# Kernel optimization log

Measured on AMD Instinct MI355X. Metric: run time of the kernel, lower is better.

Reference implementation:

```python
import jax, jax.numpy as jnp
import numpy as np

V = 8000      # output_size (vocab)
EMB = 256     # emb_size
ENC = 512     # enc_hid_size
DEC = 512     # dec_hid_size
HE = 20       # energizer hidden (fixed in source)


def setup_inputs() -> dict:
    key = jax.random.key(0)
    ks = jax.random.split(key, 12)
    B, S, T = 64, 128, 128
    s = 0.05
    return {
        "enc_hid": jax.random.normal(ks[0], (B, S, ENC), dtype=jnp.float32),
        "real_output": jax.random.randint(ks[1], (B, T), 0, V),
        "W_e1": jax.random.normal(ks[2], (ENC + DEC, HE), dtype=jnp.float32) * s,
        "b_e1": jnp.zeros((HE,), jnp.float32),
        "W_e2": jax.random.normal(ks[3], (HE, 1), dtype=jnp.float32) * s,
        "b_e2": jnp.zeros((1,), jnp.float32),
        "emb": jax.random.normal(ks[4], (V, EMB), dtype=jnp.float32) * s,
        "W_rnn": jax.random.normal(ks[5], (EMB + DEC + ENC, DEC), dtype=jnp.float32) * s,
        "b_rnn": jnp.zeros((DEC,), jnp.float32),
        "W_out": jax.random.normal(ks[6], (EMB + DEC + ENC, V), dtype=jnp.float32) * s,
        "b_out": jnp.zeros((V,), jnp.float32),
    }


def _decode(enc_hid, real_output, W_e1, b_e1, W_e2, b_e2, emb, W_rnn, b_rnn, W_out, b_out):
    B, S, _ = enc_hid.shape

    def step(carry, y_i):
        last_char, last_hidden = carry  # [B] int, [B,DEC]
        # additive attention, vectorized over all encoder positions
        hid_b = jnp.broadcast_to(last_hidden[:, None, :], (B, S, DEC))
        cat = jnp.concatenate([enc_hid, hid_b], axis=-1)          # [B,S,ENC+DEC]
        e = jax.nn.elu(cat @ W_e1 + b_e1)                          # [B,S,HE]
        e = jax.nn.elu(e @ W_e2 + b_e2)[..., 0]                    # [B,S]
        ew = jnp.exp(e)
        w = ew / jnp.sum(ew, axis=1, keepdims=True)                # [B,S]
        context = jnp.einsum('bs,bse->be', w, enc_hid)             # [B,ENC]
        last_ch = emb[last_char % V]                               # [B,EMB]
        new_hidden = jax.nn.elu(
            jnp.concatenate([last_ch, last_hidden, context], axis=1) @ W_rnn + b_rnn)
        out = jax.nn.elu(
            jnp.concatenate([last_ch, new_hidden, context], axis=1) @ W_out + b_out)
        # teacher_forcing_prob = 1.0 -> next char is the ground truth token
        return (y_i, new_hidden), (out, w)

    init = (jnp.zeros((B,), real_output.dtype), jnp.zeros((B, DEC), enc_hid.dtype))
    _, (outs, weights) = jax.lax.scan(step, init, real_output.T)   # [T,B,V], [T,B,S]
    return outs.transpose(1, 0, 2), weights.transpose(1, 0, 2)


def reference(enc_hid, real_output, W_e1, b_e1, W_e2, b_e2, emb, W_rnn, b_rnn, W_out, b_out):
    return _decode(enc_hid, real_output, W_e1, b_e1, W_e2, b_e2, emb,
                   W_rnn, b_rnn, W_out, b_out)
```

## Files before the change

### kernel.cpp

```cpp
#include <hip/hip_runtime.h>
#include <hip/hip_bf16.h>
#include <stdint.h>

#define BATCH 64
#define SLEN 128
#define TLEN 128
#define ENCD 512
#define DECD 512
#define EMBD 256
#define VOC  8000
#define HE   20
#define KX   1280
#define NPAD 8064

typedef __attribute__((ext_vector_type(8))) short short8;
typedef __attribute__((ext_vector_type(8))) _Float16 half8v;
typedef __attribute__((ext_vector_type(4))) float f32x4;
typedef _Float16 h2 __attribute__((ext_vector_type(2)));

__device__ inline unsigned short f2bf(float f) {
  union { float f; uint32_t u; } v; v.f = f;
  uint32_t r = v.u + 0x7fff + ((v.u >> 16) & 1);
  return (unsigned short)(r >> 16);
}
__device__ inline unsigned short f16bits(float f) {
  union { _Float16 h; unsigned short u; } c; c.h = (_Float16)f; return c.u;
}
__device__ inline uint32_t pkh2(float a, float b) {
  union { h2 h; uint32_t u; } v;
  v.h = h2{(_Float16)a, (_Float16)b};
  return v.u;
}
__device__ inline float fdot2(uint32_t a, uint32_t b, float c) {
#if __has_builtin(__builtin_amdgcn_fdot2)
  union { uint32_t u; h2 h; } x, y; x.u = a; y.u = b;
  return __builtin_amdgcn_fdot2(x.h, y.h, c, false);
#else
  union { uint32_t u; h2 h; } x, y; x.u = a; y.u = b;
  return c + (float)x.h[0] * (float)y.h[0] + (float)x.h[1] * (float)y.h[1];
#endif
}
__device__ inline float eluf(float x) { return x > 0.f ? x : (expf(x) - 1.f); }

typedef const __attribute__((address_space(1))) unsigned int* gptr_t;
typedef __attribute__((address_space(3))) unsigned int* lptr_t;
__device__ inline void gload16(const void* g, void* l) {
  __builtin_amdgcn_global_load_lds((gptr_t)g, (lptr_t)l, 16, 0, 0);
}

__global__ __launch_bounds__(256) void k_e1(const float* __restrict__ enc,
                                            const float* __restrict__ We1,
                                            float* __restrict__ E1) {
  __shared__ float rowbuf[4][ENCD];
  __shared__ float part[4][HE][2];
  int r0 = blockIdx.x * 4;
  int tid = threadIdx.x;
  for (int i = tid; i < 4 * ENCD; i += 256) {
    int rl = i >> 9, e = i & 511;
    rowbuf[rl][e] = enc[(size_t)(r0 + rl) * ENCD + e];
  }
  __syncthreads();
  if (tid < 160) {
    int kg = tid / 80, rem = tid % 80, rl = rem / 20, h = rem % 20;
    float acc = 0.f;
    for (int k = kg * 256; k < kg * 256 + 256; ++k)
      acc += rowbuf[rl][k] * We1[k * HE + h];
    part[rl][h][kg] = acc;
  }
  __syncthreads();
  if (tid < 80) {
    int rl = tid / 20, h = tid % 20;
    int r = r0 + rl, bb = r >> 7, ss = r & 127;
    E1[((size_t)bb * HE + h) * SLEN + ss] = part[rl][h][0] + part[rl][h][1];
  }
}

__global__ __launch_bounds__(256) void k_tr_wout(const float* __restrict__ Wo,
                                                 unsigned short* __restrict__ WoT) {
  __shared__ float tile[64][65];
  int n0 = blockIdx.x * 64, k0 = blockIdx.y * 64;
  int tid = threadIdx.x;
  for (int i = tid; i < 4096; i += 256) {
    int kk = i >> 6, nn = i & 63;
    int n = n0 + nn;
    tile[kk][nn] = (n < VOC) ? Wo[(size_t)(k0 + kk) * VOC + n] : 0.f;
  }
  __syncthreads();
  for (int i = tid; i < 4096; i += 256) {
    int nn = i >> 6, kk = i & 63;
    WoT[(size_t)(n0 + nn) * KX + k0 + kk] = f2bf(tile[kk][nn]);
  }
}

__global__ __launch_bounds__(256) void k_tr_w(const float* __restrict__ src,
                                              unsigned short* __restrict__ dst,
                                              int k0, int KN, int fmt) {
  __shared__ float tile[64][65];
  int n0 = blockIdx.x * 64, kt = blockIdx.y * 64;
  int tid = threadIdx.x;
  for (int i = tid; i < 4096; i += 256) {
    int kk = i >> 6, nn = i & 63;
    tile[kk][nn] = src[(size_t)(k0 + kt + kk) * 512 + n0 + nn];
  }
  __syncthreads();
  for (int i = tid; i < 4096; i += 256) {
    int nn = i >> 6, kk = i & 63;
    float v = tile[kk][nn];
    dst[(size_t)(n0 + nn) * KN + kt + kk] = fmt ? f2bf(v) : f16bits(v);
  }
}

__global__ __launch_bounds__(256) void k_prep_wr(const float* __restrict__ Wr,
                                                 unsigned short* __restrict__ W2) {
  int i = blockIdx.x * 256 + threadIdx.x;
  int n = i & 511;
  int j = (i >> 9) & 7;
  int kc = (i >> 12) & 31;
  int h = (i >> 17) & 1;
  int k = h * 256 + kc * 8 + j;
  W2[(((size_t)(h * 32 + kc) * 512) + n) * 8 + j] = f16bits(Wr[(size_t)(256 + k) * 512 + n]);
}

__global__ __launch_bounds__(256) void k_ench(const float* __restrict__ enc,
                                              unsigned short* __restrict__ ench) {
  int i = (blockIdx.x * 256 + threadIdx.x) * 4;
  float4 v = *(const float4*)(enc + i);
  ushort4 o = { f16bits(v.x), f16bits(v.y), f16bits(v.z), f16bits(v.w) };
  *(ushort4*)(ench + i) = o;
}

__global__ __launch_bounds__(256) void k_wh(const float* __restrict__ wout,
                                            unsigned short* __restrict__ wh) {
  int i = (blockIdx.x * 256 + threadIdx.x) * 4;
  float4 v = *(const float4*)(wout + i);
  ushort4 o = { f16bits(v.x), f16bits(v.y), f16bits(v.z), f16bits(v.w) };
  *(ushort4*)(wh + i) = o;
}

__global__ __launch_bounds__(256) void k_tr_encb(const float* __restrict__ enc,
                                                 unsigned short* __restrict__ encT) {
  __shared__ float tile[64][65];
  int b = blockIdx.x, e0 = blockIdx.y * 64, s0 = blockIdx.z * 64;
  int tid = threadIdx.x;
  const float* eb = enc + (size_t)b * SLEN * ENCD;
  for (int i = tid; i < 4096; i += 256) {
    int ss = i >> 6, ee = i & 63;
    tile[ss][ee] = eb[(size_t)(s0 + ss) * ENCD + e0 + ee];
  }
  __syncthreads();
  unsigned short* ob = encT + (size_t)b * ENCD * SLEN;
  for (int i = tid; i < 4096; i += 256) {
    int ee = i >> 6, ss = i & 63;
    ob[(size_t)(e0 + ee) * SLEN + s0 + ss] = f16bits(tile[ss][ee]);
  }
}

__global__ __launch_bounds__(256) void k_lc(const int* __restrict__ ro,
                                            const float* __restrict__ emb,
                                            unsigned short* __restrict__ X) {
  int r = blockIdx.x;
  int t = r >> 6, b = r & 63;
  int lc = (t == 0) ? 0 : ro[b * TLEN + t - 1];
  lc = ((lc % VOC) + VOC) % VOC;
  X[(size_t)r * KX + threadIdx.x] = f2bf(emb[(size_t)lc * EMBD + threadIdx.x]);
}

#define BM 128
#define BN 128
#define BK 64

template<int MODE>
__global__ __launch_bounds__(256) void k_gs(
    const unsigned short* __restrict__ A,
    const unsigned short* __restrict__ B,
    const float* __restrict__ bias,
    unsigned short* __restrict__ Cout)
{
  constexpr int As = (MODE == 0) ? KX : (MODE == 1 ? 512 : 128);
  constexpr int Bs = (MODE == 0) ? 256 : (MODE == 1 ? 512 : 128);
  constexpr int KT = (MODE == 0) ? 4 : (MODE == 1 ? 8 : 2);
  __shared__ __align__(16) unsigned short Asd[BM * BK];
  __shared__ __align__(16) unsigned short Bsd[BN * BK];
  int bx = blockIdx.x, by = blockIdx.y;
  int tid = threadIdx.x;
  int wid = tid >> 6, lane = tid & 63;
  int wr = wid >> 1, wc = wid & 1;

  f32x4 acc[4][4];
  for (int i = 0; i < 4; ++i)
    for (int j = 0; j < 4; ++j) acc[i][j] = (f32x4)0.f;

  const unsigned short* Abase = A + (size_t)by * BM * As;
  const unsigned short* Bbase = B + (size_t)bx * BN * Bs + (MODE == 2 ? (size_t)by * 512 * 128 : 0);

  for (int kt = 0; kt < KT; ++kt) {
    for (int j = 0; j < 4; ++j) {
      int c = tid + j * 256;
      int r = c >> 3, c16 = c & 7;
      int sk = c16 ^ (r & 7);
      gload16(Abase + (size_t)r * As + kt * BK + sk * 8, (char*)Asd + c * 16);
      gload16(Bbase + (size_t)r * Bs + kt * BK + sk * 8, (char*)Bsd + c * 16);
    }
    __syncthreads();
    for (int ks = 0; ks < 2; ++ks) {
      short8 af[4], bf[4];
      int kc = ks * 4 + (lane >> 4);
      for (int i = 0; i < 4; ++i) {
        int r = wr * 64 + i * 16 + (lane & 15);
        af[i] = *(const short8*)((const char*)Asd + r * 128 + ((kc ^ (r & 7)) * 16));
      }
      for (int j = 0; j < 4; ++j) {
        int r = wc * 64 + j * 16 + (lane & 15);
        bf[j] = *(const short8*)((const char*)Bsd + r * 128 + ((kc ^ (r & 7)) * 16));
      }
      for (int i = 0; i < 4; ++i)
        for (int j = 0; j < 4; ++j) {
          if constexpr (MODE == 0)
            acc[i][j] = __builtin_amdgcn_mfma_f32_16x16x32_bf16(af[i], bf[j], acc[i][j], 0, 0, 0);
          else
            acc[i][j] = __builtin_amdgcn_mfma_f32_16x16x32_f16(
                __builtin_bit_cast(half8v, af[i]), __builtin_bit_cast(half8v, bf[j]), acc[i][j], 0, 0, 0);
        }
    }
    __syncthreads();
  }

  int rl = lane >> 4, cl = lane & 15;
  for (int j = 0; j < 4; ++j) {
    int gn = bx * BN + wc * 64 + j * 16 + cl;
    for (int i = 0; i < 4; ++i) {
      for (int q = 0; q < 4; ++q) {
        int gm = by * BM + wr * 64 + i * 16 + rl * 4 + q;
        float v = acc[i][j][q];
        if constexpr (MODE == 0) {
          Cout[(size_t)gm * 512 + gn] = f16bits(v + bias[gn]);
        } else if constexpr (MODE == 1) {
          int bb = gm >> 7, s = gm & 127;
          Cout[(((size_t)(bb * 16 + (s >> 3)) * 512) + gn) * 8 + (s & 7)] = f16bits(v);
        } else {
          int tt = gm & 127, bb = gm >> 7;
          Cout[((size_t)tt * 64 + bb) * KX + 768 + gn] = f2bf(v);
        }
      }
    }
  }
}

__global__ __launch_bounds__(1024) void k_recur(
    const float* __restrict__ We1,
    const float* __restrict__ be1,
    const float* __restrict__ We2,
    const float* __restrict__ be2,
    const uint4* __restrict__ W2,
    const uint4* __restrict__ encW2,
    const unsigned short* __restrict__ Remb,
    const float* __restrict__ E1g,
    unsigned short* __restrict__ X,
    float* __restrict__ wout)
{
  __shared__ __align__(16) uint4 el[16][512];
  __shared__ uint32_t E1p[HE][SLEN / 2];
  __shared__ uint32_t w1p[HE][257];
  __shared__ uint32_t hpair[DECD / 2];
  __shared__ uint32_t wpairS[SLEN / 2];
  __shared__ float ph[2][DECD];
  __shared__ float be1s[HE], w2s[HE];
  __shared__ float be2s;

  int b = blockIdx.x, tid = threadIdx.x;

  for (int i = tid; i < 16 * 512; i += 1024) ((uint4*)el)[i] = encW2[(size_t)b * 8192 + i];
  for (int i = tid; i < HE * (SLEN / 2); i += 1024) {
    int h = i >> 6, p = i & 63;
    const float* ebase = E1g + ((size_t)b * HE + h) * SLEN;
    ((uint32_t*)E1p)[i] = pkh2(ebase[2 * p], ebase[2 * p + 1]);
  }
  for (int i = tid; i < HE * 256; i += 1024) {
    int h = i >> 8, p = i & 255;
    w1p[h][p] = pkh2(We1[(size_t)(ENCD + 2 * p) * HE + h],
                     We1[(size_t)(ENCD + 2 * p + 1) * HE + h]);
  }
  for (int i = tid; i < DECD / 2; i += 1024) hpair[i] = 0;
  for (int i = tid; i < DECD; i += 1024) { ph[0][i] = 0.f; ph[1][i] = 0.f; }
  if (tid < HE) { be1s[tid] = be1[tid]; w2s[tid] = We2[tid]; }
  if (tid == 0) be2s = be2[0];
  __syncthreads();

  const int lane = tid & 63;
  const bool attn_wave = (tid >= 960);
  int mn, mh0, mblocks;
  if (tid < 448)      { mn = tid;              mh0 = 0; mblocks = 4; }
  else if (tid < 896) { mn = tid - 448;        mh0 = 1; mblocks = 4; }
  else if (tid < 960) { mn = 448 + (tid - 896); mh0 = 0; mblocks = 8; }
  else                { mn = 0;                mh0 = 0; mblocks = 0; }
  const uint4* Wp = W2 + (size_t)(mh0 * 32) * 512 + mn;
  const uint4* hp4 = (const uint4*)hpair;
  const int hbase = mh0 * 32;

  int ah = lane % 20, aseg = lane / 20;
  int q0 = aseg * 86;
  int q1 = (aseg == 2) ? 256 : q0 + 86;
  if (aseg >= 3) { q0 = 0; q1 = 0; }

  for (int t = 0; t < TLEN; ++t) {
    const int rowr = t * BATCH + b;
    float rpre = 0.f;

    if (!attn_wave) {
      if (tid < 512) {
        union { unsigned short u; _Float16 f; } c;
        c.u = Remb[(size_t)rowr * 512 + tid];
        rpre = (float)c.f;
      }
      float a0 = 0, a1 = 0, a2 = 0, a3 = 0;
      uint4 cb[8], nb[8];
      #pragma unroll
      for (int j = 0; j < 8; ++j) cb[j] = Wp[(size_t)j * 512];
      for (int blk = 0; blk < mblocks; ++blk) {
        if (blk + 1 < mblocks) {
          #pragma unroll
          for (int j = 0; j < 8; ++j) nb[j] = Wp[(size_t)((blk + 1) * 8 + j) * 512];
        }
        #pragma unroll
        for (int j = 0; j < 8; ++j) {
          uint4 wv = cb[j]; uint4 xv = hp4[hbase + blk * 8 + j];
          a0 = fdot2(wv.x, xv.x, a0); a1 = fdot2(wv.y, xv.y, a1);
          a2 = fdot2(wv.z, xv.z, a2); a3 = fdot2(wv.w, xv.w, a3);
        }
        #pragma unroll
        for (int j = 0; j < 8; ++j) cb[j] = nb[j];
      }
      ph[mh0][mn] = (a0 + a1) + (a2 + a3);
    } else {
      float p0 = 0, p1 = 0;
      for (int q = q0; q < q1; q += 2) {
        p0 = fdot2(w1p[ah][q], hpair[q], p0);
        p1 = fdot2(w1p[ah][q + 1], hpair[q + 1], p1);
      }
      float p = p0 + p1;
      float pa = __shfl(p, lane + 20);
      float pb = __shfl(p, lane + 40);
      float edv = p + pa + pb + ((lane < HE) ? be1s[lane] : 0.f);
      float e0a = 0.f, e1a = 0.f;
      #pragma unroll
      for (int h = 0; h < HE; ++h) {
        union { uint32_t u; h2 hh; } e; e.u = E1p[h][lane];
        float ed = __shfl(edv, h);
        e0a += eluf((float)e.hh[0] + ed) * w2s[h];
        e1a += eluf((float)e.hh[1] + ed) * w2s[h];
      }
      float s0 = expf(eluf(e0a + be2s));
      float s1 = expf(eluf(e1a + be2s));
      float tot = s0 + s1;
      #pragma unroll
      for (int o = 1; o < 64; o <<= 1) tot += __shfl_xor(tot, o);
      float inv = 1.f / tot;
      float w0 = s0 * inv, w1 = s1 * inv;
      wpairS[lane] = pkh2(w0, w1);
      float2 wv2 = { w0, w1 };
      *(float2*)(wout + ((size_t)b * TLEN + t) * SLEN + 2 * lane) = wv2;
    }
    __syncthreads();

    if (tid < 512) {
      int n = tid;
      float c0 = 0, c1 = 0, c2 = 0, c3 = 0;
      #pragma unroll
      for (int g = 0; g < 16; ++g) {
        uint4 ev = el[g][n];
        uint4 wv = ((const uint4*)wpairS)[g];
        c0 = fdot2(ev.x, wv.x, c0); c1 = fdot2(ev.y, wv.y, c1);
        c2 = fdot2(ev.z, wv.z, c2); c3 = fdot2(ev.w, wv.w, c3);
      }
      float v = rpre + ph[0][n] + ph[1][n] + (c0 + c1) + (c2 + c3);
      float aa = eluf(v);
      X[(size_t)rowr * KX + 256 + n] = f2bf(aa);
      float bb = __shfl_down(aa, 1);
      if (!(n & 1)) hpair[n >> 1] = pkh2(aa, bb);
    }
    __syncthreads();
  }
}

__global__ __launch_bounds__(256) void k_gemm(
    const unsigned short* __restrict__ Xb,
    const unsigned short* __restrict__ WoT,
    const float* __restrict__ bout,
    float* __restrict__ out)
{
  __shared__ __align__(16) unsigned short As[BM * BK];
  __shared__ __align__(16) unsigned short Bs[BN * BK];
  int bx = blockIdx.x;
  int by = blockIdx.y;
  int tid = threadIdx.x;
  int wid = tid >> 6, lane = tid & 63;
  int wr = wid >> 1, wc = wid & 1;

  f32x4 acc[4][4];
  for (int i = 0; i < 4; ++i)
    for (int j = 0; j < 4; ++j) acc[i][j] = (f32x4)0.f;

  const unsigned short* Abase = Xb + (size_t)by * BM * KX;
  const unsigned short* Bbase = WoT + (size_t)bx * BN * KX;

  for (int kt = 0; kt < KX / BK; ++kt) {
    for (int j = 0; j < 4; ++j) {
      int c = tid + j * 256;
      int r = c >> 3, c16 = c & 7;
      int sk = c16 ^ (r & 7);
      gload16(Abase + (size_t)r * KX + kt * BK + sk * 8, (char*)As + c * 16);
      gload16(Bbase + (size_t)r * KX + kt * BK + sk * 8, (char*)Bs + c * 16);
    }
    __syncthreads();
    for (int ks = 0; ks < 2; ++ks) {
      short8 af[4], bf[4];
      int kc = ks * 4 + (lane >> 4);
      for (int i = 0; i < 4; ++i) {
        int r = wr * 64 + i * 16 + (lane & 15);
        af[i] = *(const short8*)((const char*)As + r * 128 + ((kc ^ (r & 7)) * 16));
      }
      for (int j = 0; j < 4; ++j) {
        int r = wc * 64 + j * 16 + (lane & 15);
        bf[j] = *(const short8*)((const char*)Bs + r * 128 + ((kc ^ (r & 7)) * 16));
      }
      for (int i = 0; i < 4; ++i)
        for (int j = 0; j < 4; ++j)
          acc[i][j] = __builtin_amdgcn_mfma_f32_16x16x32_bf16(af[i], bf[j], acc[i][j], 0, 0, 0);
    }
    __syncthreads();
  }

  int rl = lane >> 4, cl = lane & 15;
  for (int j = 0; j < 4; ++j) {
    int gn = bx * BN + wc * 64 + j * 16 + cl;
    if (gn >= VOC) continue;
    float bv = bout[gn];
    for (int i = 0; i < 4; ++i) {
      for (int q = 0; q < 4; ++q) {
        int gm = by * BM + wr * 64 + i * 16 + rl * 4 + q;
        int tt = gm >> 6, bb = gm & 63;
        float v = acc[i][j][q] + bv;
        v = v > 0.f ? v : (expf(v) - 1.f);
        out[((size_t)bb * TLEN + tt) * VOC + gn] = v;
      }
    }
  }
}

extern "C" void kernel_launch(void* const* d_in, const int* in_sizes, int n_in,
                              void* d_out, int out_size, void* d_ws, size_t ws_size,
                              hipStream_t stream) {
  const float* enc  = (const float*)d_in[0];
  const int*   ro   = (const int*)d_in[1];
  const float* We1  = (const float*)d_in[2];
  const float* be1  = (const float*)d_in[3];
  const float* We2  = (const float*)d_in[4];
  const float* be2  = (const float*)d_in[5];
  const float* emb  = (const float*)d_in[6];
  const float* Wr   = (const float*)d_in[7];
  const float* brnn = (const float*)d_in[8];
  const float* Wo   = (const float*)d_in[9];
  const float* bo   = (const float*)d_in[10];

  char* ws = (char*)d_ws;
  unsigned short* X     = (unsigned short*)(ws);
  unsigned short* WoT   = (unsigned short*)(ws + 20971520);
  unsigned short* W2    = (unsigned short*)(ws + 41615360);
  unsigned short* WembT = (unsigned short*)(ws + 42139648);
  unsigned short* WctxT = (unsigned short*)(ws + 42401792);
  unsigned short* ench  = (unsigned short*)(ws + 42926080);
  float*          E1    = (float*)(ws + 51314688);
  unsigned short* Remb  = (unsigned short*)(ws + 51970048);
  unsigned short* encW2 = (unsigned short*)(ws + 60358656);
  unsigned short* encTh = ench;
  unsigned short* wh    = Remb;

  float* outs = (float*)d_out;
  float* wout = (float*)d_out + (size_t)BATCH * TLEN * VOC;

  k_lc     <<<dim3(8192),     256, 0, stream>>>(ro, emb, X);
  k_e1     <<<dim3(2048),     256, 0, stream>>>(enc, We1, E1);
  k_tr_wout<<<dim3(126, 20),  256, 0, stream>>>(Wo, WoT);
  k_tr_w   <<<dim3(8, 4),     256, 0, stream>>>(Wr, WembT, 0, 256, 1);
  k_tr_w   <<<dim3(8, 8),     256, 0, stream>>>(Wr, WctxT, 768, 512, 0);
  k_prep_wr<<<dim3(1024),     256, 0, stream>>>(Wr, W2);
  k_ench   <<<dim3(4096),     256, 0, stream>>>(enc, ench);
  k_gs<0>  <<<dim3(4, 64),    256, 0, stream>>>(X, WembT, brnn, Remb);
  k_gs<1>  <<<dim3(4, 64),    256, 0, stream>>>(ench, WctxT, brnn, encW2);
  k_recur  <<<dim3(64),      1024, 0, stream>>>(We1, be1, We2, be2,
                                                (const uint4*)W2, (const uint4*)encW2,
                                                Remb, E1, X, wout);
  k_wh     <<<dim3(1024),     256, 0, stream>>>(wout, wh);
  k_tr_encb<<<dim3(64, 8, 2), 256, 0, stream>>>(enc, encTh);
  k_gs<2>  <<<dim3(4, 64),    256, 0, stream>>>(wh, encTh, brnn, X);
  k_gemm   <<<dim3(63, 64),   256, 0, stream>>>(X, WoT, bo, outs);
  (void)in_sizes; (void)n_in; (void)out_size; (void)ws_size;
}
```

Baseline: 1.436 ms.

## Split hidden-state matvec evenly across all waves and overlap with attention

```diff
diff --git a/kernel.cpp b/kernel.cpp
--- a/kernel.cpp
+++ b/kernel.cpp
@@ -246,7 +246,15 @@
   }
 }
 
-__global__ __launch_bounds__(1024) void k_recur(
+#define LOADW(BUF, G) { _Pragma("unroll") \
+  for (int j = 0; j < 8; ++j) BUF[j] = Wp[(size_t)((G) * 8 + j) * 512]; }
+#define CONSW(BUF, G) { _Pragma("unroll") \
+  for (int j = 0; j < 8; ++j) { \
+    uint4 wv = BUF[j]; uint4 xv = hp4[hbase + (G) * 8 + j]; \
+    a0 = fdot2(wv.x, xv.x, a0); a1 = fdot2(wv.y, xv.y, a1); \
+    a2 = fdot2(wv.z, xv.z, a2); a3 = fdot2(wv.w, xv.w, a3); } }
+
+__global__ __launch_bounds__(1024, 1) void k_recur(
     const float* __restrict__ We1,
     const float* __restrict__ be1,
     const float* __restrict__ We2,
@@ -288,11 +296,7 @@
 
   const int lane = tid & 63;
   const bool attn_wave = (tid >= 960);
-  int mn, mh0, mblocks;
-  if (tid < 448)      { mn = tid;              mh0 = 0; mblocks = 4; }
-  else if (tid < 896) { mn = tid - 448;        mh0 = 1; mblocks = 4; }
-  else if (tid < 960) { mn = 448 + (tid - 896); mh0 = 0; mblocks = 8; }
-  else                { mn = 0;                mh0 = 0; mblocks = 0; }
+  const int mh0 = tid >> 9, mn = tid & 511;
   const uint4* Wp = W2 + (size_t)(mh0 * 32) * 512 + mn;
   const uint4* hp4 = (const uint4*)hpair;
   const int hbase = mh0 * 32;
@@ -304,34 +308,18 @@
 
   for (int t = 0; t < TLEN; ++t) {
     const int rowr = t * BATCH + b;
+
     float rpre = 0.f;
-
-    if (!attn_wave) {
-      if (tid < 512) {
-        union { unsigned short u; _Float16 f; } c;
-        c.u = Remb[(size_t)rowr * 512 + tid];
-        rpre = (float)c.f;
-      }
-      float a0 = 0, a1 = 0, a2 = 0, a3 = 0;
-      uint4 cb[8], nb[8];
-      #pragma unroll
-      for (int j = 0; j < 8; ++j) cb[j] = Wp[(size_t)j * 512];
-      for (int blk = 0; blk < mblocks; ++blk) {
-        if (blk + 1 < mblocks) {
-          #pragma unroll
-          for (int j = 0; j < 8; ++j) nb[j] = Wp[(size_t)((blk + 1) * 8 + j) * 512];
-        }
-        #pragma unroll
-        for (int j = 0; j < 8; ++j) {
-          uint4 wv = cb[j]; uint4 xv = hp4[hbase + blk * 8 + j];
-          a0 = fdot2(wv.x, xv.x, a0); a1 = fdot2(wv.y, xv.y, a1);
-          a2 = fdot2(wv.z, xv.z, a2); a3 = fdot2(wv.w, xv.w, a3);
-        }
-        #pragma unroll
-        for (int j = 0; j < 8; ++j) cb[j] = nb[j];
-      }
-      ph[mh0][mn] = (a0 + a1) + (a2 + a3);
-    } else {
+    if (tid < 512) {
+      union { unsigned short u; _Float16 f; } c;
+      c.u = Remb[(size_t)rowr * 512 + tid];
+      rpre = (float)c.f;
+    }
+    float a0 = 0, a1 = 0, a2 = 0, a3 = 0;
+    uint4 bA[8], bB[8];
+    LOADW(bA, 0) LOADW(bB, 1)
+
+    if (attn_wave) {
       float p0 = 0, p1 = 0;
       for (int q = q0; q < q1; q += 2) {
         p0 = fdot2(w1p[ah][q], hpair[q], p0);
@@ -360,6 +348,12 @@
       float2 wv2 = { w0, w1 };
       *(float2*)(wout + ((size_t)b * TLEN + t) * SLEN + 2 * lane) = wv2;
     }
+
+    CONSW(bA, 0) LOADW(bA, 2)
+    CONSW(bB, 1) LOADW(bB, 3)
+    CONSW(bA, 2)
+    CONSW(bB, 3)
+    ph[mh0][mn] = (a0 + a1) + (a2 + a3);
     __syncthreads();
 
     if (tid < 512) {
```

Result: slower. 1.654 ms (+15.2%).
